# Optimization experiments

Measured on AMD Instinct MI355X. Metric: run time of the kernel, lower is better.

The kernel has to match this reference:

```python
import jax, jax.numpy as jnp
import numpy as np


def setup_inputs() -> dict:
    key = jax.random.key(0)
    x = jax.random.normal(key, (32, 256, 64, 64), dtype=jnp.float32)
    return {"x": x}


def reference(x) -> jnp.ndarray:
    # x: [B, 4*C, H, W] with per-channel subband packing x[:, c*4+k] = (cA,cH,cV,cD)
    B, C4, H, W = x.shape
    C = C4 // 4
    xs = x.reshape(B, C, 4, H, W)
    cA, cH, cV, cD = xs[:, :, 0], xs[:, :, 1], xs[:, :, 2], xs[:, :, 3]
    # pywt haar idwt2: exact 2x2 block synthesis (orthonormal haar, scale 1/2)
    half = jnp.float32(0.5)
    o00 = (cA + cH + cV + cD) * half  # out[2i,   2j]
    o01 = (cA + cH - cV - cD) * half  # out[2i,   2j+1]
    o10 = (cA - cH + cV - cD) * half  # out[2i+1, 2j]
    o11 = (cA - cH - cV + cD) * half  # out[2i+1, 2j+1]
    # interleave columns then rows (depth-to-space)
    row0 = jnp.stack([o00, o01], axis=-1).reshape(B, C, H, 2 * W)
    row1 = jnp.stack([o10, o11], axis=-1).reshape(B, C, H, 2 * W)
    out = jnp.stack([row0, row1], axis=-2).reshape(B, C, 2 * H, 2 * W)
    return out
```

## Files before the change

### kernel.cpp

```cpp
#include <hip/hip_runtime.h>


#define NTHREAD 1024
#define NBLOCK  4096

typedef float f32x2 __attribute__((ext_vector_type(2)));
typedef float f32x4 __attribute__((ext_vector_type(4)));

__global__ __launch_bounds__(NTHREAD) void iwt_kernel(const f32x2* __restrict__ xv,
                                                      f32x4* __restrict__ ov) {
    int tid = blockIdx.x * NTHREAD + threadIdx.x;

    int base = ((tid >> 11) << 13) + (((tid >> 5) & 63) << 5) + (tid & 31);
    f32x2 a  = xv[base];
    f32x2 hh = xv[base + 2048];
    f32x2 v  = xv[base + 4096];
    f32x2 d  = xv[base + 6144];

    float px = a.x + d.x, qx = a.x - d.x, rx = hh.x + v.x, sx = hh.x - v.x;
    float py = a.y + d.y, qy = a.y - d.y, ry = hh.y + v.y, sy = hh.y - v.y;

    f32x4 r0, r1;
    r0.x = (px + rx) * 0.5f;  r0.y = (qx + sx) * 0.5f;
    r0.z = (py + ry) * 0.5f;  r0.w = (qy + sy) * 0.5f;
    r1.x = (qx - sx) * 0.5f;  r1.y = (px - rx) * 0.5f;
    r1.z = (qy - sy) * 0.5f;  r1.w = (py - ry) * 0.5f;

    int ob = ((tid >> 11) << 12) + (((tid >> 5) & 63) << 6) + (tid & 31);
    ov[ob]      = r0;
    ov[ob + 32] = r1;
}

extern "C" void kernel_launch(void* const* d_in, const int* in_sizes, int n_in,
                              void* d_out, int out_size, void* d_ws, size_t ws_size,
                              hipStream_t stream) {
    const f32x2* x = (const f32x2*)d_in[0];
    f32x4* out = (f32x4*)d_out;

    iwt_kernel<<<NBLOCK, NTHREAD, 0, stream>>>(x, out);
}
```

Baseline: 223.5 us.

## Stage per-channel input tile into LDS via direct global-to-LDS loads

Each block now handles one (batch, channel) group. It copies the 64KB of four subbands into shared memory with global_load_lds 16-byte transfers, then computes the 2x2 synthesis from LDS over eight row iterations per thread. The aim is fully coalesced wide loads that bypass registers and more bytes in flight per block. In exchange it uses 64KB of LDS per block, which limits occupancy, and adds a block-wide barrier between load and compute with no overlap.

```diff
diff --git a/kernel.cpp b/kernel.cpp
--- a/kernel.cpp
+++ b/kernel.cpp
@@ -1,40 +1,65 @@
 #include <hip/hip_runtime.h>
 
 
-#define NTHREAD 1024
-#define NBLOCK  4096
+#define NTHREAD 256
+#define NBLOCK  2048
 
 typedef float f32x2 __attribute__((ext_vector_type(2)));
 typedef float f32x4 __attribute__((ext_vector_type(4)));
 
-__global__ __launch_bounds__(NTHREAD) void iwt_kernel(const f32x2* __restrict__ xv,
+__global__ __launch_bounds__(NTHREAD) void iwt_kernel(const float* __restrict__ x,
                                                       f32x4* __restrict__ ov) {
-    int tid = blockIdx.x * NTHREAD + threadIdx.x;
+    __shared__ float lds[16384];
 
-    int base = ((tid >> 11) << 13) + (((tid >> 5) & 63) << 5) + (tid & 31);
-    f32x2 a  = xv[base];
-    f32x2 hh = xv[base + 2048];
-    f32x2 v  = xv[base + 4096];
-    f32x2 d  = xv[base + 6144];
+    const int bc   = blockIdx.x;
+    const int wave = threadIdx.x >> 6;
+    const int lane = threadIdx.x & 63;
 
-    float px = a.x + d.x, qx = a.x - d.x, rx = hh.x + v.x, sx = hh.x - v.x;
-    float py = a.y + d.y, qy = a.y - d.y, ry = hh.y + v.y, sy = hh.y - v.y;
+    const char* gbase = (const char*)x + ((size_t)bc << 16);
+    char* lbase = (char*)lds;
+    #pragma unroll
+    for (int t = 0; t < 16; ++t) {
+        int off = (((t << 2) + wave) << 10) + (lane << 4);
+        __builtin_amdgcn_global_load_lds(
+            (const __attribute__((address_space(1))) unsigned int*)(gbase + off),
+            (__attribute__((address_space(3))) unsigned int*)(lbase + off),
+            16, 0, 0);
+    }
+    __syncthreads();
 
-    f32x4 r0, r1;
-    r0.x = (px + rx) * 0.5f;  r0.y = (qx + sx) * 0.5f;
-    r0.z = (py + ry) * 0.5f;  r0.w = (qy + sy) * 0.5f;
-    r1.x = (qx - sx) * 0.5f;  r1.y = (px - rx) * 0.5f;
-    r1.z = (qy - sy) * 0.5f;  r1.w = (py - ry) * 0.5f;
+    const f32x2* l2 = (const f32x2*)lds;
+    f32x4* ob = ov + (bc << 12);
+    const int w2 = threadIdx.x & 31;
+    const int hb = threadIdx.x >> 5;
 
-    int ob = ((tid >> 11) << 12) + (((tid >> 5) & 63) << 6) + (tid & 31);
-    ov[ob]      = r0;
-    ov[ob + 32] = r1;
+    #pragma unroll
+    for (int k = 0; k < 8; ++k) {
+        int h  = hb + (k << 3);
+        int li = (h << 5) + w2;
+        f32x2 a  = l2[li];
+        f32x2 hh = l2[li + 2048];
+        f32x2 v  = l2[li + 4096];
+        f32x2 d  = l2[li + 6144];
+
+        float px = a.x + d.x, qx = a.x - d.x, rx = hh.x + v.x, sx = hh.x - v.x;
+        float py = a.y + d.y, qy = a.y - d.y, ry = hh.y + v.y, sy = hh.y - v.y;
+
+        f32x4 r0, r1;
+        r0.x = (px + rx) * 0.5f;  r0.y = (qx + sx) * 0.5f;
+        r0.z = (py + ry) * 0.5f;  r0.w = (qy + sy) * 0.5f;
+        r1.x = (qx - sx) * 0.5f;  r1.y = (px - rx) * 0.5f;
+        r1.z = (qy - sy) * 0.5f;  r1.w = (py - ry) * 0.5f;
+
+        int oo = (h << 6) + w2;
+        ob[oo]      = r0;
+        ob[oo + 32] = r1;
+    }
 }
 
 extern "C" void kernel_launch(void* const* d_in, const int* in_sizes, int n_in,
                               void* d_out, int out_size, void* d_ws, size_t ws_size,
                               hipStream_t stream) {
-    const f32x2* x = (const f32x2*)d_in[0];
+    const float* x = (const float*)d_in[0];
     f32x4* out = (f32x4*)d_out;
 
     iwt_kernel<<<NBLOCK, NTHREAD, 0, stream>>>(x, out);
```

Result: slower. 232.1 us (+3.8%).
